# Kernel optimization log

Measured on AMD Instinct MI355X. Metric: run time of the kernel, lower is better.

The kernel has to match this reference:

```python
import jax, jax.numpy as jnp
import numpy as np

N_NODES = 50000
N_EDGES = 1_600_000
N_GRAPHS = 64
EMB = 1280
GCN_DIMS = [128, 256, 256]
FC_DIMS = [1024, 128]
EPS = 1e-5  # BatchNorm eps (torch default)


def setup_inputs() -> dict:
    key = jax.random.key(0)
    ks = jax.random.split(key, 16)
    inp = {}
    inp["x"] = jax.random.normal(ks[0], (N_NODES, EMB), jnp.float32)
    inp["edge_index"] = jax.random.randint(ks[1], (2, N_EDGES), 0, N_NODES)
    inp["batch"] = jnp.sort(jax.random.randint(ks[2], (N_NODES,), 0, N_GRAPHS))
    dims = [EMB] + GCN_DIMS
    for i in range(3):
        inp[f"Wg{i}"] = jax.random.normal(ks[3 + i], (dims[i], dims[i + 1]), jnp.float32) * (1.0 / np.sqrt(dims[i]))
        inp[f"bg{i}"] = jnp.zeros((dims[i + 1],), jnp.float32)
        inp[f"gamma{i}"] = jnp.ones((dims[i + 1],), jnp.float32)
        inp[f"beta{i}"] = jnp.zeros((dims[i + 1],), jnp.float32)
    fdims = [GCN_DIMS[-1]] + FC_DIMS
    for i in range(2):
        inp[f"Wf{i}"] = jax.random.normal(ks[10 + i], (fdims[i], fdims[i + 1]), jnp.float32) * (1.0 / np.sqrt(fdims[i]))
        inp[f"bf{i}"] = jnp.zeros((fdims[i + 1],), jnp.float32)
    return inp


def _batchnorm(h, gamma, beta):
    # training-mode BN over node dim, biased variance (torch normalization)
    m = h.mean(axis=0)
    v = h.var(axis=0)
    return gamma * (h - m) * jax.lax.rsqrt(v + EPS) + beta


def reference(x, edge_index, batch,
              Wg0, bg0, gamma0, beta0,
              Wg1, bg1, gamma1, beta1,
              Wg2, bg2, gamma2, beta2,
              Wf0, bf0, Wf1, bf1):
    # --- GCN symmetric normalization with self-loops (PyG GCNConv default) ---
    loop = jnp.arange(N_NODES)
    src = jnp.concatenate([edge_index[0], loop])  # message sources
    dst = jnp.concatenate([edge_index[1], loop])  # aggregation targets
    deg = jax.ops.segment_sum(jnp.ones(src.shape[0], jnp.float32), dst, num_segments=N_NODES)
    dinv = jnp.where(deg > 0, jax.lax.rsqrt(jnp.maximum(deg, 1.0)), 0.0)
    norm = dinv[src] * dinv[dst]  # [E + N]

    def gcn_conv(h, W, b):
        h = h @ W                               # [N, d_out] transform first (PyG order)
        msg = h[src] * norm[:, None]            # gather + scale
        return jax.ops.segment_sum(msg, dst, num_segments=N_NODES) + b

    h = x
    for W, b, g, bt in ((Wg0, bg0, gamma0, beta0),
                        (Wg1, bg1, gamma1, beta1),
                        (Wg2, bg2, gamma2, beta2)):
        h = gcn_conv(h, W, b)
        h = _batchnorm(h, g, bt)
        h = jax.nn.relu(h)
        # dropout is identity in eval mode

    # --- global mean pool over graphs ---
    counts = jax.ops.segment_sum(jnp.ones(N_NODES, jnp.float32), batch, num_segments=N_GRAPHS)
    sums = jax.ops.segment_sum(h, batch, num_segments=N_GRAPHS)
    g = sums / jnp.maximum(counts, 1.0)[:, None]  # [B, 256]

    # --- FC head ---
    g = jax.nn.relu(g @ Wf0 + bf0)
    out = g @ Wf1 + bf1                           # [B, 128]
    return out
```

## Files before the change

kernel.cpp:

```cpp
#include <hip/hip_runtime.h>
#include <hip/hip_bf16.h>

#define N_NODES 50000
#define N_EDGES 1600000
#define N_GRAPHS 64

typedef _Float16 f16;
typedef _Float16 f16x8 __attribute__((ext_vector_type(8)));
typedef _Float16 f16x4 __attribute__((ext_vector_type(4)));
typedef _Float16 f16x2 __attribute__((ext_vector_type(2)));
typedef float f32x4 __attribute__((ext_vector_type(4)));

template <int V> struct VecT;
template <> struct VecT<2> { using type = f16x2; };
template <> struct VecT<4> { using type = f16x4; };

__global__ void init_deg(int* deg) {
    int i = blockIdx.x * blockDim.x + threadIdx.x;
    if (i < N_NODES) deg[i] = 1;
}

__global__ void deg_count(const int* __restrict__ dst, int* __restrict__ deg) {
    int e = blockIdx.x * blockDim.x + threadIdx.x;
    if (e < N_EDGES) atomicAdd(&deg[dst[e]], 1);
}

__global__ void make_dinv(const int* __restrict__ deg, float* __restrict__ dinv) {
    int i = blockIdx.x * blockDim.x + threadIdx.x;
    if (i < N_NODES) dinv[i] = rsqrtf((float)deg[i]);
}

__global__ void scan_deg(const int* __restrict__ deg, int* __restrict__ rowstart,
                         int* __restrict__ pos) {
    __shared__ int wsum[16];
    __shared__ int carry_s;
    const int t = threadIdx.x;
    const int lane = t & 63;
    const int w = t >> 6;
    if (t == 0) carry_s = 0;
    __syncthreads();
    for (int base = 0; base < N_NODES; base += 1024) {
        int i = base + t;
        int v = (i < N_NODES) ? (deg[i] - 1) : 0;
        int s = v;
#pragma unroll
        for (int off = 1; off < 64; off <<= 1) {
            int n = __shfl_up(s, off, 64);
            if (lane >= off) s += n;
        }
        if (lane == 63) wsum[w] = s;
        __syncthreads();
        if (w == 0) {
            int ws = (lane < 16) ? wsum[lane] : 0;
#pragma unroll
            for (int off = 1; off < 16; off <<= 1) {
                int n = __shfl_up(ws, off, 64);
                if (lane >= off) ws += n;
            }
            if (lane < 16) wsum[lane] = ws;
        }
        __syncthreads();
        int waveoff = (w == 0) ? 0 : wsum[w - 1];
        int carry = carry_s;
        int excl = carry + waveoff + s - v;
        if (i < N_NODES) {
            rowstart[i] = excl;
            pos[i] = excl;
        }
        __syncthreads();
        if (t == 0) carry_s = carry + wsum[15];
        __syncthreads();
    }
    if (t == 0) rowstart[N_NODES] = carry_s;
}

__global__ void csr_fill(const int* __restrict__ src, const int* __restrict__ dst,
                         const float* __restrict__ dinv, int* __restrict__ pos,
                         int2* __restrict__ csr) {
    int e = blockIdx.x * blockDim.x + threadIdx.x;
    if (e >= N_EDGES) return;
    int s = src[e], d = dst[e];
    int slot = atomicAdd(&pos[d], 1);
    csr[slot] = make_int2(s, __float_as_int(dinv[s] * dinv[d]));
}

__global__ void cast_w(const float* __restrict__ W, f16* __restrict__ Wt, int K, int N) {
    int i = blockIdx.x * blockDim.x + threadIdx.x;
    if (i >= K * N) return;
    int k = i % K, n = i / K;
    Wt[i] = (f16)W[(size_t)k * N + n];
}

__launch_bounds__(256)
__global__ void gemm_x_sk_pipe(const float* __restrict__ A, const f16* __restrict__ Bt,
                               float* __restrict__ C0, float* __restrict__ C1, int M) {
    const int K = 1280, KC = 640;
    const int gw = (int)((blockIdx.x * blockDim.x + threadIdx.x) >> 6);
    const int lane = threadIdx.x & 63;
    const int tile = gw >> 1, s = gw & 1;
    const int m0 = tile * 32;
    if (m0 >= M) return;
    float* __restrict__ C = s ? C1 : C0;
    const int kbeg = s * KC;
    const int r = lane & 15, q = lane >> 4;
    int row0 = m0 + r;       row0 = row0 < M ? row0 : M - 1;
    int row1 = m0 + 16 + r;  row1 = row1 < M ? row1 : M - 1;
    const float* a0 = A + (size_t)row0 * K + kbeg + q * 8;
    const float* a1 = A + (size_t)row1 * K + kbeg + q * 8;
    const f16* bp = Bt + (size_t)r * K + kbeg + q * 8;

    f32x4 acc[2][8];
#pragma unroll
    for (int i = 0; i < 2; ++i)
#pragma unroll
        for (int j = 0; j < 8; ++j) acc[i][j] = (f32x4){0.f, 0.f, 0.f, 0.f};

    float4 ab[2][4];
    f16x8 bb[2][8];
    ab[0][0] = *(const float4*)(a0);
    ab[0][1] = *(const float4*)(a0 + 4);
    ab[0][2] = *(const float4*)(a1);
    ab[0][3] = *(const float4*)(a1 + 4);
#pragma unroll
    for (int ni = 0; ni < 8; ++ni) bb[0][ni] = *(const f16x8*)(bp + (size_t)ni * 16 * K);

#pragma unroll
    for (int kt = 0; kt < 20; ++kt) {
        const int cur = kt & 1, nxt = cur ^ 1;
        if (kt < 19) {
            const int ko = (kt + 1) * 32;
            ab[nxt][0] = *(const float4*)(a0 + ko);
            ab[nxt][1] = *(const float4*)(a0 + ko + 4);
            ab[nxt][2] = *(const float4*)(a1 + ko);
            ab[nxt][3] = *(const float4*)(a1 + ko + 4);
#pragma unroll
            for (int ni = 0; ni < 8; ++ni)
                bb[nxt][ni] = *(const f16x8*)(bp + (size_t)ni * 16 * K + ko);
        }
        f16x8 af0 = {(f16)ab[cur][0].x, (f16)ab[cur][0].y, (f16)ab[cur][0].z, (f16)ab[cur][0].w,
                     (f16)ab[cur][1].x, (f16)ab[cur][1].y, (f16)ab[cur][1].z, (f16)ab[cur][1].w};
        f16x8 af1 = {(f16)ab[cur][2].x, (f16)ab[cur][2].y, (f16)ab[cur][2].z, (f16)ab[cur][2].w,
                     (f16)ab[cur][3].x, (f16)ab[cur][3].y, (f16)ab[cur][3].z, (f16)ab[cur][3].w};
#pragma unroll
        for (int ni = 0; ni < 8; ++ni) {
            acc[0][ni] = __builtin_amdgcn_mfma_f32_16x16x32_f16(af0, bb[cur][ni], acc[0][ni], 0, 0, 0);
            acc[1][ni] = __builtin_amdgcn_mfma_f32_16x16x32_f16(af1, bb[cur][ni], acc[1][ni], 0, 0, 0);
        }
    }
#pragma unroll
    for (int mi = 0; mi < 2; ++mi)
#pragma unroll
        for (int j = 0; j < 4; ++j) {
            int row = m0 + mi * 16 + q * 4 + j;
            if (row < M) {
                float* cp = C + (size_t)row * 128 + r;
#pragma unroll
                for (int ni = 0; ni < 8; ++ni) cp[ni * 16] = acc[mi][ni][j];
            }
        }
}

__global__ void reduce_cast(const float* __restrict__ c0, const float* __restrict__ c1,
                            f16* __restrict__ o, int n4) {
    int i = blockIdx.x * blockDim.x + threadIdx.x;
    if (i >= n4) return;
    float4 a = ((const float4*)c0)[i];
    float4 b = ((const float4*)c1)[i];
    f16x4 r = {(f16)(a.x + b.x), (f16)(a.y + b.y), (f16)(a.z + b.z), (f16)(a.w + b.w)};
    ((f16x4*)o)[i] = r;
}

template <int K>
__launch_bounds__(256)
__global__ void gemm_h_bn_pipe(const f16* __restrict__ A16, const float* __restrict__ ss,
                               const f16* __restrict__ Bt, f16* __restrict__ C16, int N) {
    constexpr int NT = K / 32;
    const int gw = (int)((blockIdx.x * blockDim.x + threadIdx.x) >> 6);
    const int lane = threadIdx.x & 63;
    const int m0 = gw * 32;
    if (m0 >= N_NODES) return;
    const int col0 = blockIdx.y * 128;
    const int r = lane & 15, q = lane >> 4;
    int row0 = m0 + r;       row0 = row0 < N_NODES ? row0 : N_NODES - 1;
    int row1 = m0 + 16 + r;  row1 = row1 < N_NODES ? row1 : N_NODES - 1;
    const f16* a0 = A16 + (size_t)row0 * K + q * 8;
    const f16* a1 = A16 + (size_t)row1 * K + q * 8;
    const f16* bp = Bt + (size_t)(col0 + r) * K + q * 8;
    const float* scp = ss + q * 8;
    const float* shp = ss + K + q * 8;

    f32x4 acc[2][8];
#pragma unroll
    for (int i = 0; i < 2; ++i)
#pragma unroll
        for (int j = 0; j < 8; ++j) acc[i][j] = (f32x4){0.f, 0.f, 0.f, 0.f};

    f16x8 ab[2][2];
    f16x8 bb[2][8];
    float4 sb[2][4];
    ab[0][0] = *(const f16x8*)(a0);
    ab[0][1] = *(const f16x8*)(a1);
    sb[0][0] = *(const float4*)(scp);
    sb[0][1] = *(const float4*)(scp + 4);
    sb[0][2] = *(const float4*)(shp);
    sb[0][3] = *(const float4*)(shp + 4);
#pragma unroll
    for (int ni = 0; ni < 8; ++ni) bb[0][ni] = *(const f16x8*)(bp + (size_t)ni * 16 * K);

#pragma unroll
    for (int kt = 0; kt < NT; ++kt) {
        const int cur = kt & 1, nxt = cur ^ 1;
        if (kt < NT - 1) {
            const int ko = (kt + 1) * 32;
            ab[nxt][0] = *(const f16x8*)(a0 + ko);
            ab[nxt][1] = *(const f16x8*)(a1 + ko);
            sb[nxt][0] = *(const float4*)(scp + ko);
            sb[nxt][1] = *(const float4*)(scp + ko + 4);
            sb[nxt][2] = *(const float4*)(shp + ko);
            sb[nxt][3] = *(const float4*)(shp + ko + 4);
#pragma unroll
            for (int ni = 0; ni < 8; ++ni)
                bb[nxt][ni] = *(const f16x8*)(bp + (size_t)ni * 16 * K + ko);
        }
        float sc[8] = {sb[cur][0].x, sb[cur][0].y, sb[cur][0].z, sb[cur][0].w,
                       sb[cur][1].x, sb[cur][1].y, sb[cur][1].z, sb[cur][1].w};
        float sh[8] = {sb[cur][2].x, sb[cur][2].y, sb[cur][2].z, sb[cur][2].w,
                       sb[cur][3].x, sb[cur][3].y, sb[cur][3].z, sb[cur][3].w};
        f16x8 af0, af1;
#pragma unroll
        for (int j = 0; j < 8; ++j) {
            float v0 = (float)ab[cur][0][j] * sc[j] + sh[j];
            float v1 = (float)ab[cur][1][j] * sc[j] + sh[j];
            af0[j] = (f16)(v0 > 0.f ? v0 : 0.f);
            af1[j] = (f16)(v1 > 0.f ? v1 : 0.f);
        }
#pragma unroll
        for (int ni = 0; ni < 8; ++ni) {
            acc[0][ni] = __builtin_amdgcn_mfma_f32_16x16x32_f16(af0, bb[cur][ni], acc[0][ni], 0, 0, 0);
            acc[1][ni] = __builtin_amdgcn_mfma_f32_16x16x32_f16(af1, bb[cur][ni], acc[1][ni], 0, 0, 0);
        }
    }
#pragma unroll
    for (int mi = 0; mi < 2; ++mi)
#pragma unroll
        for (int j = 0; j < 4; ++j) {
            int row = m0 + mi * 16 + q * 4 + j;
            if (row < N_NODES) {
                f16* cp = C16 + (size_t)row * N + col0 + r;
#pragma unroll
                for (int ni = 0; ni < 8; ++ni) cp[ni * 16] = (f16)acc[mi][ni][j];
            }
        }
}

template <int D>
__launch_bounds__(256)
__global__ void aggregate(const f16* __restrict__ h, const int* __restrict__ rowstart,
                          const int2* __restrict__ csr, const float* __restrict__ dinv,
                          const float* __restrict__ bias, f16* __restrict__ out) {
    constexpr int V = D / 64;
    using vec = typename VecT<V>::type;
    int w = (int)((blockIdx.x * blockDim.x + threadIdx.x) >> 6);
    int lane = threadIdx.x & 63;
    if (w >= N_NODES) return;
    float acc[V];
    float di = dinv[w];
    vec self = *(const vec*)(h + (size_t)w * D + lane * V);
#pragma unroll
    for (int v = 0; v < V; ++v) acc[v] = (float)self[v] * (di * di);
    int e0 = rowstart[w], e1 = rowstart[w + 1];
    int j = e0;
    for (; j + 8 <= e1; j += 8) {
        int2 c[8];
        vec rr[8];
#pragma unroll
        for (int u = 0; u < 8; ++u) c[u] = csr[j + u];
#pragma unroll
        for (int u = 0; u < 8; ++u)
            rr[u] = *(const vec*)(h + (size_t)c[u].x * D + lane * V);
#pragma unroll
        for (int u = 0; u < 8; ++u) {
            float nm = __int_as_float(c[u].y);
#pragma unroll
            for (int v = 0; v < V; ++v) acc[v] += (float)rr[u][v] * nm;
        }
    }
    if (j + 4 <= e1) {
        int2 c0 = csr[j], c1 = csr[j + 1], c2 = csr[j + 2], c3 = csr[j + 3];
        vec r0 = *(const vec*)(h + (size_t)c0.x * D + lane * V);
        vec r1 = *(const vec*)(h + (size_t)c1.x * D + lane * V);
        vec r2 = *(const vec*)(h + (size_t)c2.x * D + lane * V);
        vec r3 = *(const vec*)(h + (size_t)c3.x * D + lane * V);
        float n0 = __int_as_float(c0.y), n1 = __int_as_float(c1.y);
        float n2 = __int_as_float(c2.y), n3 = __int_as_float(c3.y);
#pragma unroll
        for (int v = 0; v < V; ++v)
            acc[v] += (float)r0[v] * n0 + (float)r1[v] * n1 +
                      (float)r2[v] * n2 + (float)r3[v] * n3;
        j += 4;
    }
    for (; j < e1; ++j) {
        int2 c = csr[j];
        vec r = *(const vec*)(h + (size_t)c.x * D + lane * V);
        float nm = __int_as_float(c.y);
#pragma unroll
        for (int v = 0; v < V; ++v) acc[v] += (float)r[v] * nm;
    }
    vec o;
#pragma unroll
    for (int v = 0; v < V; ++v) o[v] = (f16)(acc[v] + bias[lane * V + v]);
    *(vec*)(out + (size_t)w * D + lane * V) = o;
}

template <int D>
__global__ void bn_stats(const f16* __restrict__ h, float* __restrict__ stat) {
    int f = threadIdx.x;
    int r0 = blockIdx.x * 128;
    int r1 = min(r0 + 128, N_NODES);
    float s = 0.f, s2 = 0.f;
    for (int r = r0; r < r1; ++r) {
        float v = (float)h[(size_t)r * D + f];
        s += v;
        s2 += v * v;
    }
    atomicAdd(&stat[f], s);
    atomicAdd(&stat[D + f], s2);
}

template <int D>
__global__ void bn_finalize(const float* __restrict__ stat, const float* __restrict__ gamma,
                            const float* __restrict__ beta, float* __restrict__ ss) {
    int f = threadIdx.x;
    float m = stat[f] * (1.0f / N_NODES);
    float var = stat[D + f] * (1.0f / N_NODES) - m * m;
    float sc = gamma[f] * rsqrtf(var + 1e-5f);
    ss[f] = sc;
    ss[D + f] = beta[f] - m * sc;
}

__global__ void count_batch_bs(const int* __restrict__ batch, int* __restrict__ cnt) {
    int g = threadIdx.x;
    if (g >= N_GRAPHS) return;
    int lo = 0, hi = N_NODES;
    while (lo < hi) { int mid = (lo + hi) >> 1; if (batch[mid] < g) lo = mid + 1; else hi = mid; }
    int b0 = lo;
    lo = 0; hi = N_NODES;
    while (lo < hi) { int mid = (lo + hi) >> 1; if (batch[mid] < g + 1) lo = mid + 1; else hi = mid; }
    cnt[g] = lo - b0;
}

__global__ void pool_seg_bn(const f16* __restrict__ h, const float* __restrict__ ss,
                            const int* __restrict__ batch, float* __restrict__ psum) {
    int f = threadIdx.x;
    float sc = ss[f], sh = ss[256 + f];
    int r0 = blockIdx.x * 64;
    int r1 = min(r0 + 64, N_NODES);
    float acc = 0.f;
    int cur = batch[r0];
    for (int r = r0; r < r1; ++r) {
        int b = batch[r];
        if (b != cur) {
            atomicAdd(&psum[cur * 256 + f], acc);
            acc = 0.f;
            cur = b;
        }
        float v = sc * (float)h[(size_t)r * 256 + f] + sh;
        acc += v > 0.f ? v : 0.f;
    }
    atomicAdd(&psum[cur * 256 + f], acc);
}

__global__ void pool_div(const float* __restrict__ psum, const int* __restrict__ cnt,
                         float* __restrict__ g) {
    int i = blockIdx.x * 256 + threadIdx.x;
    int b = i >> 8;
    float c = (float)max(cnt[b], 1);
    g[i] = psum[i] / c;
}

__global__ void fc_init(const float* __restrict__ b, float* __restrict__ Y, int rows, int N) {
    int i = blockIdx.x * blockDim.x + threadIdx.x;
    if (i < rows * N) Y[i] = b[i % N];
}

__global__ void fc_splitk(const float* __restrict__ X, const float* __restrict__ W,
                          float* __restrict__ Y, int K, int N, int KC) {
    int col = blockIdx.x * blockDim.x + threadIdx.x;
    int row = blockIdx.y;
    int k0 = blockIdx.z * KC;
    float acc = 0.f;
    const float* x = X + (size_t)row * K + k0;
    const float* w = W + (size_t)k0 * N + col;
#pragma unroll 8
    for (int k = 0; k < KC; ++k) acc += x[k] * w[(size_t)k * N];
    atomicAdd(&Y[(size_t)row * N + col], acc);
}

__global__ void relu_inplace(float* __restrict__ Y, int n) {
    int i = blockIdx.x * blockDim.x + threadIdx.x;
    if (i < n) Y[i] = Y[i] > 0.f ? Y[i] : 0.f;
}

extern "C" void kernel_launch(void* const* d_in, const int* in_sizes, int n_in,
                              void* d_out, int out_size, void* d_ws, size_t ws_size,
                              hipStream_t stream) {
    const float* x     = (const float*)d_in[0];
    const int*   ei    = (const int*)d_in[1];
    const int*   batch = (const int*)d_in[2];
    const float* Wg0 = (const float*)d_in[3],  *bg0 = (const float*)d_in[4];
    const float* gamma0 = (const float*)d_in[5], *beta0 = (const float*)d_in[6];
    const float* Wg1 = (const float*)d_in[7],  *bg1 = (const float*)d_in[8];
    const float* gamma1 = (const float*)d_in[9], *beta1 = (const float*)d_in[10];
    const float* Wg2 = (const float*)d_in[11], *bg2 = (const float*)d_in[12];
    const float* gamma2 = (const float*)d_in[13], *beta2 = (const float*)d_in[14];
    const float* Wf0 = (const float*)d_in[15], *bf0 = (const float*)d_in[16];
    const float* Wf1 = (const float*)d_in[17], *bf1 = (const float*)d_in[18];
    float* out = (float*)d_out;

    size_t off = 0;
    auto alloc = [&](size_t bytes) {
        void* p = (char*)d_ws + off;
        off += (bytes + 255) & ~(size_t)255;
        return p;
    };
    f16*   hA16     = (f16*)alloc((size_t)N_NODES * 256 * 2);
    float* cp32     = (float*)alloc((size_t)2 * N_NODES * 128 * 4);
    f16*   hBn16    = (f16*)cp32;
    float* cp0      = cp32;
    float* cp1      = cp32 + (size_t)N_NODES * 128;
    int2*  csr      = (int2*)alloc((size_t)N_EDGES * 8);
    int*   deg      = (int*)alloc((size_t)N_NODES * 4);
    float* dinv     = (float*)alloc((size_t)N_NODES * 4);
    int*   rowstart = (int*)alloc((size_t)(N_NODES + 1) * 4);
    int*   pos      = (int*)alloc((size_t)N_NODES * 4);
    float* bnstat   = (float*)alloc(2 * 256 * 4);
    float* bnss     = (float*)alloc(2 * 256 * 4);
    float* psum     = (float*)alloc(64 * 256 * 4);
    int*   pcount   = (int*)alloc(64 * 4);
    float* gpool    = (float*)alloc(64 * 256 * 4);
    float* g1       = (float*)alloc(64 * 1024 * 4);
    f16*   W0t      = (f16*)alloc((size_t)1280 * 128 * 2);
    f16*   W1t      = (f16*)alloc((size_t)128 * 256 * 2);
    f16*   W2t      = (f16*)alloc((size_t)256 * 256 * 2);
    (void)ws_size;

    const int TPB = 256;
    const int nb_nodes = (N_NODES + TPB - 1) / TPB;
    const int nb_edges = (N_EDGES + TPB - 1) / TPB;

    init_deg<<<nb_nodes, TPB, 0, stream>>>(deg);
    deg_count<<<nb_edges, TPB, 0, stream>>>(ei + N_EDGES, deg);
    make_dinv<<<nb_nodes, TPB, 0, stream>>>(deg, dinv);
    scan_deg<<<1, 1024, 0, stream>>>(deg, rowstart, pos);
    csr_fill<<<nb_edges, TPB, 0, stream>>>(ei, ei + N_EDGES, dinv, pos, csr);
    cast_w<<<(1280 * 128 + 255) / 256, 256, 0, stream>>>(Wg0, W0t, 1280, 128);
    cast_w<<<(128 * 256 + 255) / 256, 256, 0, stream>>>(Wg1, W1t, 128, 256);
    cast_w<<<(256 * 256 + 255) / 256, 256, 0, stream>>>(Wg2, W2t, 256, 256);

    const int gemm0_blocks = (1563 * 2 * 64 + TPB - 1) / TPB;
    const int gemmh_blocks = (1563 * 64 + TPB - 1) / TPB;
    const int agg_blocks = (N_NODES * 64 + TPB - 1) / TPB;

    gemm_x_sk_pipe<<<gemm0_blocks, TPB, 0, stream>>>(x, W0t, cp0, cp1, N_NODES);
    reduce_cast<<<(N_NODES * 128 / 4 + 255) / 256, 256, 0, stream>>>(cp0, cp1, hA16, N_NODES * 128 / 4);
    aggregate<128><<<agg_blocks, TPB, 0, stream>>>(hA16, rowstart, csr, dinv, bg0, hBn16);
    hipMemsetAsync(bnstat, 0, 2 * 128 * 4, stream);
    bn_stats<128><<<(N_NODES + 127) / 128, 128, 0, stream>>>(hBn16, bnstat);
    bn_finalize<128><<<1, 128, 0, stream>>>(bnstat, gamma0, beta0, bnss);

    gemm_h_bn_pipe<128><<<dim3(gemmh_blocks, 2), TPB, 0, stream>>>(hBn16, bnss, W1t, hA16, 256);
    aggregate<256><<<agg_blocks, TPB, 0, stream>>>(hA16, rowstart, csr, dinv, bg1, hBn16);
    hipMemsetAsync(bnstat, 0, 2 * 256 * 4, stream);
    bn_stats<256><<<(N_NODES + 127) / 128, 256, 0, stream>>>(hBn16, bnstat);
    bn_finalize<256><<<1, 256, 0, stream>>>(bnstat, gamma1, beta1, bnss);

    gemm_h_bn_pipe<256><<<dim3(gemmh_blocks, 2), TPB, 0, stream>>>(hBn16, bnss, W2t, hA16, 256);
    aggregate<256><<<agg_blocks, TPB, 0, stream>>>(hA16, rowstart, csr, dinv, bg2, hBn16);
    hipMemsetAsync(bnstat, 0, 2 * 256 * 4, stream);
    bn_stats<256><<<(N_NODES + 127) / 128, 256, 0, stream>>>(hBn16, bnstat);
    bn_finalize<256><<<1, 256, 0, stream>>>(bnstat, gamma2, beta2, bnss);

    hipMemsetAsync(psum, 0, 64 * 256 * 4, stream);
    count_batch_bs<<<1, 64, 0, stream>>>(batch, pcount);
    pool_seg_bn<<<(N_NODES + 63) / 64, 256, 0, stream>>>(hBn16, bnss, batch, psum);
    pool_div<<<64, 256, 0, stream>>>(psum, pcount, gpool);

    fc_init<<<(64 * 1024 + 255) / 256, 256, 0, stream>>>(bf0, g1, 64, 1024);
    fc_splitk<<<dim3(4, 64, 4), 256, 0, stream>>>(gpool, Wf0, g1, 256, 1024, 64);
    relu_inplace<<<(64 * 1024 + 255) / 256, 256, 0, stream>>>(g1, 64 * 1024);
    fc_init<<<(64 * 128 + 255) / 256, 256, 0, stream>>>(bf1, out, 64, 128);
    fc_splitk<<<dim3(1, 64, 16), 128, 0, stream>>>(g1, Wf1, out, 1024, 128, 64);
}
```

Before: 895.3 us.

## Stage A tiles through LDS with direct global-to-LDS loads in first GEMM

Rewrites the first GEMM (x @ W0) so each 256-thread block covers 128 rows and stages fp32 A tiles into swizzled LDS using global_load_lds, replacing per-wave register double-buffered global loads. The intent is fully coalesced 16-byte A loads and fewer bank conflicts on the largest input read. In exchange it drops the software prefetch pipeline, adds two block barriers per k-step, and loads B fragments inline without prefetching, so latency may be exposed.

```diff
diff --git a/kernel.cpp b/kernel.cpp
--- a/kernel.cpp
+++ b/kernel.cpp
@@ -14,6 +14,12 @@
 template <int V> struct VecT;
 template <> struct VecT<2> { using type = f16x2; };
 template <> struct VecT<4> { using type = f16x4; };
+
+typedef __attribute__((address_space(3))) void lds_void_t;
+typedef const __attribute__((address_space(1))) void gbl_void_t;
+__device__ __forceinline__ void gload_lds16(const void* g, void* l) {
+    __builtin_amdgcn_global_load_lds((gbl_void_t*)g, (lds_void_t*)l, 16, 0, 0);
+}
 
 __global__ void init_deg(int* deg) {
     int i = blockIdx.x * blockDim.x + threadIdx.x;
@@ -92,21 +98,29 @@
 }
 
 __launch_bounds__(256)
-__global__ void gemm_x_sk_pipe(const float* __restrict__ A, const f16* __restrict__ Bt,
-                               float* __restrict__ C0, float* __restrict__ C1, int M) {
-    const int K = 1280, KC = 640;
-    const int gw = (int)((blockIdx.x * blockDim.x + threadIdx.x) >> 6);
-    const int lane = threadIdx.x & 63;
-    const int tile = gw >> 1, s = gw & 1;
-    const int m0 = tile * 32;
-    if (m0 >= M) return;
+__global__ void gemm_x_lds(const float* __restrict__ A, const f16* __restrict__ Bt,
+                           float* __restrict__ C0, float* __restrict__ C1, int M) {
+    const int K = 1280;
+    __shared__ float Asm[128 * 32];
+    const int t = threadIdx.x;
+    const int w = t >> 6, lane = t & 63;
+    const int tile = blockIdx.x >> 1, s = blockIdx.x & 1;
+    const int m0 = tile * 128;
+    const int kbeg = s * 640;
     float* __restrict__ C = s ? C1 : C0;
-    const int kbeg = s * KC;
     const int r = lane & 15, q = lane >> 4;
-    int row0 = m0 + r;       row0 = row0 < M ? row0 : M - 1;
-    int row1 = m0 + 16 + r;  row1 = row1 < M ? row1 : M - 1;
-    const float* a0 = A + (size_t)row0 * K + kbeg + q * 8;
-    const float* a1 = A + (size_t)row1 * K + kbeg + q * 8;
+
+    const int rl_base = w * 32 + (lane >> 3);
+    const int gchunk = (lane & 7) ^ ((lane >> 3) & 7);
+
+    const int row_l0 = w * 32 + r;
+    const int row_l1 = w * 32 + 16 + r;
+    const int sw = r & 7;
+    const float* lr0a = Asm + row_l0 * 32 + (((2 * q) ^ sw) << 2);
+    const float* lr0b = Asm + row_l0 * 32 + (((2 * q + 1) ^ sw) << 2);
+    const float* lr1a = Asm + row_l1 * 32 + (((2 * q) ^ sw) << 2);
+    const float* lr1b = Asm + row_l1 * 32 + (((2 * q + 1) ^ sw) << 2);
+
     const f16* bp = Bt + (size_t)r * K + kbeg + q * 8;
 
     f32x4 acc[2][8];
@@ -115,43 +129,38 @@
 #pragma unroll
         for (int j = 0; j < 8; ++j) acc[i][j] = (f32x4){0.f, 0.f, 0.f, 0.f};
 
-    float4 ab[2][4];
-    f16x8 bb[2][8];
-    ab[0][0] = *(const float4*)(a0);
-    ab[0][1] = *(const float4*)(a0 + 4);
-    ab[0][2] = *(const float4*)(a1);
-    ab[0][3] = *(const float4*)(a1 + 4);
-#pragma unroll
-    for (int ni = 0; ni < 8; ++ni) bb[0][ni] = *(const f16x8*)(bp + (size_t)ni * 16 * K);
-
-#pragma unroll
     for (int kt = 0; kt < 20; ++kt) {
-        const int cur = kt & 1, nxt = cur ^ 1;
-        if (kt < 19) {
-            const int ko = (kt + 1) * 32;
-            ab[nxt][0] = *(const float4*)(a0 + ko);
-            ab[nxt][1] = *(const float4*)(a0 + ko + 4);
-            ab[nxt][2] = *(const float4*)(a1 + ko);
-            ab[nxt][3] = *(const float4*)(a1 + ko + 4);
-#pragma unroll
-            for (int ni = 0; ni < 8; ++ni)
-                bb[nxt][ni] = *(const f16x8*)(bp + (size_t)ni * 16 * K + ko);
-        }
-        f16x8 af0 = {(f16)ab[cur][0].x, (f16)ab[cur][0].y, (f16)ab[cur][0].z, (f16)ab[cur][0].w,
-                     (f16)ab[cur][1].x, (f16)ab[cur][1].y, (f16)ab[cur][1].z, (f16)ab[cur][1].w};
-        f16x8 af1 = {(f16)ab[cur][2].x, (f16)ab[cur][2].y, (f16)ab[cur][2].z, (f16)ab[cur][2].w,
-                     (f16)ab[cur][3].x, (f16)ab[cur][3].y, (f16)ab[cur][3].z, (f16)ab[cur][3].w};
+        const int kk = kbeg + kt * 32;
+#pragma unroll
+        for (int i = 0; i < 4; ++i) {
+            int row_g = m0 + rl_base + i * 8;
+            row_g = row_g < M ? row_g : M - 1;
+            const float* src = A + (size_t)row_g * K + kk + gchunk * 4;
+            float* dst = Asm + (w * 32 + i * 8) * 32;
+            gload_lds16(src, dst);
+        }
+        __syncthreads();
+        float4 u0 = *(const float4*)lr0a;
+        float4 v0 = *(const float4*)lr0b;
+        float4 u1 = *(const float4*)lr1a;
+        float4 v1 = *(const float4*)lr1b;
+        f16x8 af0 = {(f16)u0.x, (f16)u0.y, (f16)u0.z, (f16)u0.w,
+                     (f16)v0.x, (f16)v0.y, (f16)v0.z, (f16)v0.w};
+        f16x8 af1 = {(f16)u1.x, (f16)u1.y, (f16)u1.z, (f16)u1.w,
+                     (f16)v1.x, (f16)v1.y, (f16)v1.z, (f16)v1.w};
 #pragma unroll
         for (int ni = 0; ni < 8; ++ni) {
-            acc[0][ni] = __builtin_amdgcn_mfma_f32_16x16x32_f16(af0, bb[cur][ni], acc[0][ni], 0, 0, 0);
-            acc[1][ni] = __builtin_amdgcn_mfma_f32_16x16x32_f16(af1, bb[cur][ni], acc[1][ni], 0, 0, 0);
-        }
+            f16x8 bf = *(const f16x8*)(bp + (size_t)ni * 16 * K + kt * 32);
+            acc[0][ni] = __builtin_amdgcn_mfma_f32_16x16x32_f16(af0, bf, acc[0][ni], 0, 0, 0);
+            acc[1][ni] = __builtin_amdgcn_mfma_f32_16x16x32_f16(af1, bf, acc[1][ni], 0, 0, 0);
+        }
+        __syncthreads();
     }
 #pragma unroll
     for (int mi = 0; mi < 2; ++mi)
 #pragma unroll
         for (int j = 0; j < 4; ++j) {
-            int row = m0 + mi * 16 + q * 4 + j;
+            int row = m0 + w * 32 + mi * 16 + q * 4 + j;
             if (row < M) {
                 float* cp = C + (size_t)row * 128 + r;
 #pragma unroll
@@ -457,11 +466,12 @@
     cast_w<<<(128 * 256 + 255) / 256, 256, 0, stream>>>(Wg1, W1t, 128, 256);
     cast_w<<<(256 * 256 + 255) / 256, 256, 0, stream>>>(Wg2, W2t, 256, 256);
 
-    const int gemm0_blocks = (1563 * 2 * 64 + TPB - 1) / TPB;
+    const int tiles128 = (N_NODES + 127) / 128;
+    const int gemm0_blocks = tiles128 * 2;
     const int gemmh_blocks = (1563 * 64 + TPB - 1) / TPB;
     const int agg_blocks = (N_NODES * 64 + TPB - 1) / TPB;
 
-    gemm_x_sk_pipe<<<gemm0_blocks, TPB, 0, stream>>>(x, W0t, cp0, cp1, N_NODES);
+    gemm_x_lds<<<gemm0_blocks, TPB, 0, stream>>>(x, W0t, cp0, cp1, N_NODES);
     reduce_cast<<<(N_NODES * 128 / 4 + 255) / 256, 256, 0, stream>>>(cp0, cp1, hA16, N_NODES * 128 / 4);
     aggregate<128><<<agg_blocks, TPB, 0, stream>>>(hA16, rowstart, csr, dinv, bg0, hBn16);
     hipMemsetAsync(bnstat, 0, 2 * 128 * 4, stream);
```

Result: faster. 857.9 us (-4.2%).
